# Kernel tuning notes

Hardware: AMD Instinct MI355X
Metric: run time of the kernel (lower is better)

Reference implementation:

```python
import jax, jax.numpy as jnp
import numpy as np

DIM = 512
H = 8
HD = 64          # hidden_dim = dim // num_heads
TD = 64          # time_dim -> time features = 2*TD = 128
LIN = 1536
EPS = 1e-5

def layer_norm(x, g, b):
    mu = jnp.mean(x, axis=-1, keepdims=True)
    var = jnp.mean((x - mu) ** 2, axis=-1, keepdims=True)
    return (x - mu) * jax.lax.rsqrt(var + EPS) * g + b

def setup_inputs() -> dict:
    key = jax.random.key(0)
    ks = jax.random.split(key, 16)
    B, L = 2, 2048
    return {
        "tensor": jax.random.normal(ks[0], (B, L, DIM), jnp.float32),
        "attention_mask": jnp.ones((B, L), jnp.float32),
        "time_angle": jax.random.uniform(ks[1], (H, TD), jnp.float32),
        "head_time_delta": jax.random.uniform(ks[2], (H,), jnp.float32),
        "Qw": jax.random.normal(ks[3], (DIM, H * HD), jnp.float32) * 0.02,
        "q_bias": jnp.zeros((H * HD,), jnp.float32),
        "Kw": jax.random.normal(ks[4], (DIM, H * HD), jnp.float32) * 0.02,
        "Kb": jax.random.normal(ks[5], (H * HD,), jnp.float32) * 0.02,
        "Vw": jax.random.normal(ks[6], (DIM, H * HD), jnp.float32) * 0.02,
        "Vb": jnp.zeros((H * HD,), jnp.float32),
        "Ow": jax.random.normal(ks[7], (H * HD, DIM), jnp.float32) * 0.02,
        "Ob": jnp.zeros((DIM,), jnp.float32),
        "ln1_g": jnp.ones((DIM,), jnp.float32),
        "ln1_b": jnp.zeros((DIM,), jnp.float32),
        "Win": jax.random.normal(ks[8], (DIM, LIN), jnp.float32) * 0.02,
        "b_in": jax.random.normal(ks[9], (LIN,), jnp.float32) * 0.02,
        "Wout": jax.random.normal(ks[10], (LIN, DIM), jnp.float32) * 0.02,
        "b_out": jnp.zeros((DIM,), jnp.float32),
        "ln2_g": jnp.ones((DIM,), jnp.float32),
        "ln2_b": jnp.zeros((DIM,), jnp.float32),
    }

def reference(tensor, attention_mask, time_angle, head_time_delta, Qw, q_bias,
              Kw, Kb, Vw, Vb, Ow, Ob, ln1_g, ln1_b, Win, b_in, Wout, b_out,
              ln2_g, ln2_b):
    B, L = tensor.shape[:2]
    inv_sqrt = 1.0 / np.sqrt(HD).astype(np.float32)
    # queries: sigmoid-gated scalar weight per (b,l,h)
    q = (tensor @ Qw - jnp.exp(q_bias)).reshape(B, L, H, HD)
    q = jax.nn.sigmoid(q) / HD * attention_mask[..., None, None]  # [B,L,H,HD]
    # time features (note: source reuses time_angles for k_time too)
    t = jnp.arange(L, dtype=tensor.dtype)
    ang = (t[:, None, None] + head_time_delta[None, :, None]) * time_angle  # [L,H,TD]
    c, s = jnp.cos(ang), jnp.sin(ang)
    time = jnp.concatenate([c + s, c - s], axis=-1) * inv_sqrt  # [L,H,2TD]
    qt = q.sum(-1)[..., None] * time                            # [B,L,H,2TD]
    # (K branch is dead code in source: computed but never used)
    attn = jnp.einsum('blhd,thd->blth', qt, time)               # [B,L,L,H]
    v = (tensor @ Vw + Vb).reshape(B, L, H, HD)
    comb = jnp.einsum('blth,bthd->blhd', attn, v)               # [B,L,H,HD]
    attn_out = comb.reshape(B, L, H * HD) @ Ow + Ob
    inter = layer_norm(tensor + attn_out, ln1_g, ln1_b)         # dropout = id (eval)
    lin = jax.nn.gelu(inter @ Win + b_in, approximate=True) @ Wout + b_out
    return layer_norm(inter + lin, ln2_g, ln2_b)
```

## Files before the change

### kernel.cpp

```cpp
#include <hip/hip_runtime.h>
#include <hip/hip_bf16.h>

typedef __hip_bfloat16 bf16;
typedef __attribute__((ext_vector_type(8))) __bf16 bf16x8;
typedef __attribute__((ext_vector_type(4))) float f32x4;

#define DIM   512
#define NH    8
#define HDIM  64
#define LIND  1536
#define LSEQ  2048
#define ROWS  4096
#define TF    128
#define KCH   32

__device__ __forceinline__ float b2f(bf16 v){ return __bfloat162float(v); }
__device__ __forceinline__ void stc(float* C, size_t i, float v){ C[i] = v; }
__device__ __forceinline__ void stc(bf16*  C, size_t i, float v){ C[i] = __float2bfloat16(v); }

typedef const __attribute__((address_space(1))) unsigned int* gp1_t;
typedef __attribute__((address_space(3))) unsigned int* lp3_t;
__device__ __forceinline__ void gload16(const bf16* g, unsigned short* l) {
    __builtin_amdgcn_global_load_lds((gp1_t)(const void*)g, (lp3_t)(void*)l, 16, 0, 0);
}

__global__ __launch_bounds__(256) void setup_kernel(const float* __restrict__ tensor,
                                                    const float* __restrict__ tang,
                                                    const float* __restrict__ htd,
                                                    const float* __restrict__ Qw,
                                                    const float* __restrict__ Vw,
                                                    const float* __restrict__ Ow,
                                                    const float* __restrict__ Win,
                                                    const float* __restrict__ Wout,
                                                    bf16* __restrict__ tensorb,
                                                    bf16* __restrict__ timef,
                                                    bf16* __restrict__ timefT,
                                                    bf16* __restrict__ QwT,
                                                    bf16* __restrict__ VwT,
                                                    bf16* __restrict__ OwT,
                                                    bf16* __restrict__ WinT,
                                                    bf16* __restrict__ WoutT)
{
    int id = blockIdx.x;
    if (id < 2048) {
        int i = id * 256 + threadIdx.x;
        float4 v = ((const float4*)tensor)[i];
        bf16 t[4];
        t[0] = __float2bfloat16(v.x); t[1] = __float2bfloat16(v.y);
        t[2] = __float2bfloat16(v.z); t[3] = __float2bfloat16(v.w);
        *(uint2*)&tensorb[(size_t)i * 4] = *(uint2*)t;
        return;
    }
    if (id < 6144) {
        int idx = (id - 2048) * 256 + threadIdx.x;
        int d = idx & 63;
        int h = (idx >> 6) & 7;
        int l = idx >> 9;
        float ang = ((float)l + htd[h]) * tang[h * 64 + d];
        float s, c;
        sincosf(ang, &s, &c);
        bf16* p = timef + ((size_t)l * NH + h) * TF;
        p[d]      = __float2bfloat16((c + s) * 0.125f);
        p[d + 64] = __float2bfloat16((c - s) * 0.125f);
        return;
    }
    if (id < 10240) {
        int q = id - 6144;
        int h  = q >> 9;
        int rem = q & 511;
        int d  = rem >> 3;
        int l  = (rem & 7) * 256 + threadIdx.x;
        float ang = ((float)l + htd[h]) * tang[h * 64 + d];
        float s, c;
        sincosf(ang, &s, &c);
        timefT[((size_t)(h * 128 + d)) * LSEQ + l]      = __float2bfloat16((c + s) * 0.125f);
        timefT[((size_t)(h * 128 + d + 64)) * LSEQ + l] = __float2bfloat16((c - s) * 0.125f);
        return;
    }
    id -= 10240;
    const float* in; bf16* out; int R, C, tx, ty;
    if (id < 256)        { in = Qw;   out = QwT;   R = 512;  C = 512;  tx = id & 15; ty = id >> 4; }
    else if (id < 512)   { id -= 256;  in = Vw;   out = VwT;   R = 512;  C = 512;  tx = id & 15; ty = id >> 4; }
    else if (id < 768)   { id -= 512;  in = Ow;   out = OwT;   R = 512;  C = 512;  tx = id & 15; ty = id >> 4; }
    else if (id < 1536)  { id -= 768;  in = Win;  out = WinT;  R = 512;  C = 1536; tx = id % 48; ty = id / 48; }
    else                 { id -= 1536; in = Wout; out = WoutT; R = 1536; C = 512;  tx = id & 15; ty = id >> 4; }

    __shared__ float t[32][33];
    int bx = tx * 32, by = ty * 32;
    int x = threadIdx.x & 31, y = threadIdx.x >> 5;
    #pragma unroll
    for (int r = 0; r < 32; r += 8)
        t[y + r][x] = in[(size_t)(by + y + r) * C + bx + x];
    __syncthreads();
    #pragma unroll
    for (int r = 0; r < 32; r += 8)
        out[(size_t)(bx + y + r) * R + by + x] = __float2bfloat16(t[x][y + r]);
}


template<int BM, int BN, int EPI, typename OUTT>
__global__ __launch_bounds__(256) void gemm_big(const bf16* __restrict__ A,
                                                const bf16* __restrict__ Bt,
                                                const float* __restrict__ bias,
                                                const float* __restrict__ res,
                                                OUTT* __restrict__ C,
                                                int M, int N, int K)
{
    constexpr int RM = BM / 32, RN = BN / 32;
    constexpr int ITA = BM / 32, ITB = BN / 32;
    __shared__ unsigned short As[2][BM * 64];
    __shared__ unsigned short Bs[2][BN * 64];

    int tid  = threadIdx.x;
    int lane = tid & 63, wave = tid >> 6;
    int wr = wave >> 1, wc = wave & 1;
    int bm = blockIdx.y * BM, bn = blockIdx.x * BN;
    int l15 = lane & 15, lk = lane >> 4;

    const bf16* gA[ITA]; const bf16* gB[ITB];
    #pragma unroll
    for (int it = 0; it < ITA; ++it) {
        int e = it * 256 + tid, row = e >> 3, g = e & 7;
        gA[it] = &A[(size_t)(bm + row) * K + (g ^ (row & 7)) * 8];
    }
    #pragma unroll
    for (int it = 0; it < ITB; ++it) {
        int e = it * 256 + tid, row = e >> 3, g = e & 7;
        gB[it] = &Bt[(size_t)(bn + row) * K + (g ^ (row & 7)) * 8];
    }

    f32x4 acc[RM][RN] = {};
    int NT = K >> 6;

    #pragma unroll
    for (int it = 0; it < ITA; ++it) gload16(gA[it], &As[0][(it * 256 + tid) * 8]);
    #pragma unroll
    for (int it = 0; it < ITB; ++it) gload16(gB[it], &Bs[0][(it * 256 + tid) * 8]);
    __syncthreads();

    for (int t = 0; t < NT; ++t) {
        int cur = t & 1;
        if (t + 1 < NT) {
            #pragma unroll
            for (int it = 0; it < ITA; ++it)
                gload16(gA[it] + (t + 1) * 64, &As[cur ^ 1][(it * 256 + tid) * 8]);
            #pragma unroll
            for (int it = 0; it < ITB; ++it)
                gload16(gB[it] + (t + 1) * 64, &Bs[cur ^ 1][(it * 256 + tid) * 8]);
        }
        #pragma unroll
        for (int s = 0; s < 2; ++s) {
            bf16x8 a[RM], b[RN];
            int g8 = ((s * 4 + lk) ^ (l15 & 7)) * 8;
            #pragma unroll
            for (int m = 0; m < RM; ++m) {
                int row = wr * (BM / 2) + m * 16 + l15;
                a[m] = *(const bf16x8*)&As[cur][row * 64 + g8];
            }
            #pragma unroll
            for (int n = 0; n < RN; ++n) {
                int row = wc * (BN / 2) + n * 16 + l15;
                b[n] = *(const bf16x8*)&Bs[cur][row * 64 + g8];
            }
            #pragma unroll
            for (int m = 0; m < RM; ++m)
                #pragma unroll
                for (int n = 0; n < RN; ++n)
                    acc[m][n] = __builtin_amdgcn_mfma_f32_16x16x32_bf16(a[m], b[n], acc[m][n], 0, 0, 0);
        }
        __syncthreads();
    }

    #pragma unroll
    for (int m = 0; m < RM; ++m) {
        #pragma unroll
        for (int n = 0; n < RN; ++n) {
            int gcol = bn + wc * (BN / 2) + n * 16 + l15;
            float bs = bias[gcol];
            #pragma unroll
            for (int r = 0; r < 4; ++r) {
                int grow = bm + wr * (BM / 2) + m * 16 + lk * 4 + r;
                float x = acc[m][n][r];
                float o;
                if constexpr (EPI == 2) {
                    o = x + bs + res[(size_t)grow * N + gcol];
                } else if constexpr (EPI == 3) {
                    float t = x + bs;
                    float u = t + 0.044715f * t * t * t;
                    o = 0.5f * t * (1.0f + tanhf(0.7978845608028654f * u));
                } else {
                    o = x + bs + res[(size_t)grow * N + gcol];
                }
                stc(C, (size_t)grow * N + gcol, o);
            }
        }
    }
}

__global__ __launch_bounds__(256) void gemm_qv(const bf16* __restrict__ A,
                                               const bf16* __restrict__ Bt,
                                               const float* __restrict__ qb,
                                               const float* __restrict__ Vb,
                                               float* __restrict__ qs,
                                               bf16* __restrict__ vT)
{
    constexpr int BM = 64, BN = 128, RM = 2, RN = 4;
    __shared__ unsigned short As[2][BM * 64];
    __shared__ unsigned short Bs[2][BN * 64];
    __shared__ float qsums[2][64];

    const int K = DIM;
    int tid  = threadIdx.x;
    int lane = tid & 63, wave = tid >> 6;
    int wr = wave >> 1, wc = wave & 1;
    int bm = blockIdx.y * BM, bn = blockIdx.x * BN;
    int l15 = lane & 15, lk = lane >> 4;

    const bf16* gA[2]; const bf16* gB[4];
    #pragma unroll
    for (int it = 0; it < 2; ++it) {
        int e = it * 256 + tid, row = e >> 3, g = e & 7;
        gA[it] = &A[(size_t)(bm + row) * K + (g ^ (row & 7)) * 8];
    }
    #pragma unroll
    for (int it = 0; it < 4; ++it) {
        int e = it * 256 + tid, row = e >> 3, g = e & 7;
        gB[it] = &Bt[(size_t)(bn + row) * K + (g ^ (row & 7)) * 8];
    }

    f32x4 acc[RM][RN] = {};
    const int NT = K >> 6;

    #pragma unroll
    for (int it = 0; it < 2; ++it) gload16(gA[it], &As[0][(it * 256 + tid) * 8]);
    #pragma unroll
    for (int it = 0; it < 4; ++it) gload16(gB[it], &Bs[0][(it * 256 + tid) * 8]);
    __syncthreads();

    for (int t = 0; t < NT; ++t) {
        int cur = t & 1;
        if (t + 1 < NT) {
            #pragma unroll
            for (int it = 0; it < 2; ++it)
                gload16(gA[it] + (t + 1) * 64, &As[cur ^ 1][(it * 256 + tid) * 8]);
            #pragma unroll
            for (int it = 0; it < 4; ++it)
                gload16(gB[it] + (t + 1) * 64, &Bs[cur ^ 1][(it * 256 + tid) * 8]);
        }
        #pragma unroll
        for (int s = 0; s < 2; ++s) {
            bf16x8 a[RM], b[RN];
            int g8 = ((s * 4 + lk) ^ (l15 & 7)) * 8;
            #pragma unroll
            for (int m = 0; m < RM; ++m) {
                int row = wr * 32 + m * 16 + l15;
                a[m] = *(const bf16x8*)&As[cur][row * 64 + g8];
            }
            #pragma unroll
            for (int n = 0; n < RN; ++n) {
                int row = wc * 64 + n * 16 + l15;
                b[n] = *(const bf16x8*)&Bs[cur][row * 64 + g8];
            }
            #pragma unroll
            for (int m = 0; m < RM; ++m)
                #pragma unroll
                for (int n = 0; n < RN; ++n)
                    acc[m][n] = __builtin_amdgcn_mfma_f32_16x16x32_bf16(a[m], b[n], acc[m][n], 0, 0, 0);
        }
        __syncthreads();
    }

    if (bn < DIM) {
        float eq[RN];
        #pragma unroll
        for (int n = 0; n < RN; ++n)
            eq[n] = expf(qb[bn + wc * 64 + n * 16 + l15]);
        #pragma unroll
        for (int m = 0; m < RM; ++m) {
            #pragma unroll
            for (int r = 0; r < 4; ++r) {
                float s = 0.f;
                #pragma unroll
                for (int n = 0; n < RN; ++n) {
                    float x = acc[m][n][r] - eq[n];
                    s += 1.0f / (1.0f + expf(-x));
                }
                s *= (1.0f / 64.0f);
                #pragma unroll
                for (int off = 1; off < 16; off <<= 1) s += __shfl_xor(s, off);
                if (l15 == 0)
                    qsums[wc][wr * 32 + m * 16 + lk * 4 + r] = s;
            }
        }
        __syncthreads();
        if (tid < 128) {
            int hh = tid >> 6, row = tid & 63;
            qs[(size_t)(bm + row) * NH + (bn >> 6) + hh] = qsums[hh][row];
        }
    } else {
        #pragma unroll
        for (int m = 0; m < RM; ++m) {
            int grow0 = bm + wr * 32 + m * 16 + lk * 4;
            #pragma unroll
            for (int n = 0; n < RN; ++n) {
                int gcol = bn - DIM + wc * 64 + n * 16 + l15;
                float bs = Vb[gcol];
                bf16 tmp[4];
                #pragma unroll
                for (int r = 0; r < 4; ++r)
                    tmp[r] = __float2bfloat16(acc[m][n][r] + bs);
                *(uint2*)&vT[(size_t)gcol * ROWS + grow0] = *(uint2*)tmp;
            }
        }
    }
}

__global__ __launch_bounds__(256) void wpart_mfma(const bf16* __restrict__ timefT,
                                                  const bf16* __restrict__ vT,
                                                  float* __restrict__ wpart)
{
    __shared__ unsigned short As[128 * 64];
    __shared__ unsigned short Bs[64 * 64];

    int bh = blockIdx.x;
    int kc = blockIdx.y;
    int b = bh >> 3, h = bh & 7;
    int tid  = threadIdx.x;
    int lane = tid & 63, wave = tid >> 6;
    int wr = wave >> 1, wc = wave & 1;
    int l15 = lane & 15, lk = lane >> 4;
    int k0 = kc * 64;

    const bf16* Abase = timefT + (size_t)h * (128 * LSEQ) + k0;
    const bf16* Bbase = vT + (size_t)h * 64 * ROWS + (size_t)b * LSEQ + k0;

    #pragma unroll
    for (int it = 0; it < 4; ++it) {
        int e = it * 256 + tid, row = e >> 3, g = e & 7;
        gload16(Abase + (size_t)row * LSEQ + (g ^ (row & 7)) * 8, &As[e * 8]);
    }
    #pragma unroll
    for (int it = 0; it < 2; ++it) {
        int e = it * 256 + tid, row = e >> 3, g = e & 7;
        gload16(Bbase + (size_t)row * ROWS + (g ^ (row & 7)) * 8, &Bs[e * 8]);
    }
    __syncthreads();

    f32x4 acc[4][2] = {};
    #pragma unroll
    for (int s = 0; s < 2; ++s) {
        bf16x8 a[4], bv[2];
        int g8 = ((s * 4 + lk) ^ (l15 & 7)) * 8;
        #pragma unroll
        for (int m = 0; m < 4; ++m) {
            int row = wr * 64 + m * 16 + l15;
            a[m] = *(const bf16x8*)&As[row * 64 + g8];
        }
        #pragma unroll
        for (int n = 0; n < 2; ++n) {
            int row = wc * 32 + n * 16 + l15;
            bv[n] = *(const bf16x8*)&Bs[row * 64 + g8];
        }
        #pragma unroll
        for (int m = 0; m < 4; ++m)
            #pragma unroll
            for (int n = 0; n < 2; ++n)
                acc[m][n] = __builtin_amdgcn_mfma_f32_16x16x32_bf16(a[m], bv[n], acc[m][n], 0, 0, 0);
    }

    float* wp = wpart + ((size_t)(kc * 16 + bh)) * (HDIM * TF);
    #pragma unroll
    for (int m = 0; m < 4; ++m) {
        int gd0 = wr * 64 + m * 16 + lk * 4;
        #pragma unroll
        for (int n = 0; n < 2; ++n) {
            int ghd = wc * 32 + n * 16 + l15;
            *(f32x4*)&wp[ghd * TF + gd0] = acc[m][n];
        }
    }
}

__global__ __launch_bounds__(256) void wred_kernel(const float* __restrict__ wpart,
                                                   bf16* __restrict__ WT)
{
    int i = blockIdx.x * 256 + threadIdx.x;
    float s = 0.f;
    #pragma unroll
    for (int kc = 0; kc < KCH; ++kc)
        s += wpart[(size_t)kc * 131072 + i];
    WT[i] = __float2bfloat16(s);
}

__global__ __launch_bounds__(256) void comb_mfma(const bf16* __restrict__ timef,
                                                 const bf16* __restrict__ WT,
                                                 const float* __restrict__ qs,
                                                 const float* __restrict__ mask,
                                                 bf16* __restrict__ comb)
{
    int bh = blockIdx.x;
    int b = bh >> 3, h = bh & 7;
    int lane = threadIdx.x & 63, wave = threadIdx.x >> 6;
    int l15 = lane & 15, lk = lane >> 4;
    int lbase = blockIdx.y * 128 + wave * 32;

    const bf16* wt = WT + (size_t)bh * (HDIM * TF);

    f32x4 acc[2][4] = {};
    #pragma unroll
    for (int ks = 0; ks < 4; ++ks) {
        int kt = ks * 32;
        bf16x8 a[2], bf[4];
        #pragma unroll
        for (int m = 0; m < 2; ++m) {
            int l = lbase + m * 16 + l15;
            a[m] = *(const bf16x8*)&timef[((size_t)l * NH + h) * TF + kt + lk * 8];
        }
        #pragma unroll
        for (int n = 0; n < 4; ++n)
            bf[n] = *(const bf16x8*)&wt[(size_t)(n * 16 + l15) * TF + kt + lk * 8];
        #pragma unroll
        for (int m = 0; m < 2; ++m)
            #pragma unroll
            for (int n = 0; n < 4; ++n)
                acc[m][n] = __builtin_amdgcn_mfma_f32_16x16x32_bf16(a[m], bf[n], acc[m][n], 0, 0, 0);
    }

    #pragma unroll
    for (int m = 0; m < 2; ++m) {
        #pragma unroll
        for (int r = 0; r < 4; ++r) {
            int l = lbase + m * 16 + lk * 4 + r;
            int row = b * LSEQ + l;
            float q = qs[(size_t)row * NH + h] * mask[row];
            #pragma unroll
            for (int n = 0; n < 4; ++n) {
                int hd = n * 16 + l15;
                comb[(size_t)row * DIM + h * HDIM + hd] =
                    __float2bfloat16(q * acc[m][n][r]);
            }
        }
    }
}

template<int WB>
__global__ __launch_bounds__(256) void ln_kernel(const float* __restrict__ X,
                                                 const float* __restrict__ g,
                                                 const float* __restrict__ bta,
                                                 float* __restrict__ outf,
                                                 bf16* __restrict__ outb)
{
    int row = blockIdx.x;
    const float* x = X + (size_t)row * DIM;
    float v0 = x[threadIdx.x], v1 = x[threadIdx.x + 256];
    float s = v0 + v1, s2 = v0 * v0 + v1 * v1;
    #pragma unroll
    for (int off = 1; off < 64; off <<= 1) {
        s  += __shfl_xor(s,  off);
        s2 += __shfl_xor(s2, off);
    }
    __shared__ float sh[2][4];
    int wave = threadIdx.x >> 6, lane = threadIdx.x & 63;
    if (lane == 0) { sh[0][wave] = s; sh[1][wave] = s2; }
    __syncthreads();
    s  = sh[0][0] + sh[0][1] + sh[0][2] + sh[0][3];
    s2 = sh[1][0] + sh[1][1] + sh[1][2] + sh[1][3];
    float mu  = s * (1.0f / DIM);
    float var = s2 * (1.0f / DIM) - mu * mu;
    float inv = rsqrtf(var + 1e-5f);
    int c0 = threadIdx.x, c1 = threadIdx.x + 256;
    float o0 = (v0 - mu) * inv * g[c0] + bta[c0];
    float o1 = (v1 - mu) * inv * g[c1] + bta[c1];
    outf[(size_t)row * DIM + c0] = o0;
    outf[(size_t)row * DIM + c1] = o1;
    if constexpr (WB) {
        outb[(size_t)row * DIM + c0] = __float2bfloat16(o0);
        outb[(size_t)row * DIM + c1] = __float2bfloat16(o1);
    }
}

extern "C" void kernel_launch(void* const* d_in, const int* in_sizes, int n_in,
                              void* d_out, int out_size, void* d_ws, size_t ws_size,
                              hipStream_t stream)
{
    const float* tensor = (const float*)d_in[0];
    const float* mask   = (const float*)d_in[1];
    const float* tang   = (const float*)d_in[2];
    const float* htd    = (const float*)d_in[3];
    const float* Qw     = (const float*)d_in[4];
    const float* qb     = (const float*)d_in[5];
    const float* Vw     = (const float*)d_in[8];
    const float* Vb     = (const float*)d_in[9];
    const float* Ow     = (const float*)d_in[10];
    const float* Ob     = (const float*)d_in[11];
    const float* g1     = (const float*)d_in[12];
    const float* b1     = (const float*)d_in[13];
    const float* Win    = (const float*)d_in[14];
    const float* bin    = (const float*)d_in[15];
    const float* Wout   = (const float*)d_in[16];
    const float* bout   = (const float*)d_in[17];
    const float* g2     = (const float*)d_in[18];
    const float* b2     = (const float*)d_in[19];
    float* out = (float*)d_out;

    float* ws = (float*)d_ws;
    bf16*  vT     = (bf16*)(ws + 0);
    bf16*  actb   = (bf16*)(ws + 0);
    bf16*  tensorb= (bf16*)(ws + 1048576);
    bf16*  combb  = tensorb;
    bf16*  timefb = (bf16*)(ws + 2097152);
    bf16*  timefT = (bf16*)(ws + 3145728);
    bf16*  interb = (bf16*)(ws + 3145728);
    float* wpart  = ws + 4194304;
    float* preLN1 = ws + 4194304;
    float* buf5   = ws + 6291456;
    float* inter  = ws + 8388608;
    bf16*  WTb    = (bf16*)(ws + 10485760);
    float* qs     = ws + 10551296;
    bf16*  QVwT   = (bf16*)(ws + 10584064);
    bf16*  QwT    = QVwT;
    bf16*  VwT    = QVwT + (size_t)512 * 512;
    bf16*  OwT    = (bf16*)(ws + 10846208);
    bf16*  WinT   = (bf16*)(ws + 10977280);
    bf16*  WoutT  = (bf16*)(ws + 11370496);

    setup_kernel<<<12544, 256, 0, stream>>>(tensor, tang, htd, Qw, Vw, Ow, Win, Wout,
                                            tensorb, timefb, timefT, QwT, VwT, OwT, WinT, WoutT);
    gemm_qv<<<dim3(8, 64), 256, 0, stream>>>(tensorb, QVwT, qb, Vb, qs, vT);
    wpart_mfma<<<dim3(16, KCH), 256, 0, stream>>>(timefT, vT, wpart);
    wred_kernel<<<512, 256, 0, stream>>>(wpart, WTb);
    comb_mfma<<<dim3(16, 16), 256, 0, stream>>>(timefb, WTb, qs, mask, combb);
    gemm_big<64, 64, 2, float><<<dim3(8, 64), 256, 0, stream>>>(combb, OwT, Ob, tensor, preLN1, ROWS, DIM, DIM);
    ln_kernel<1><<<ROWS, 256, 0, stream>>>(preLN1, g1, b1, inter, interb);
    gemm_big<64, 128, 3, bf16><<<dim3(12, 64), 256, 0, stream>>>(interb, WinT, bin, nullptr, actb, ROWS, LIND, DIM);
    gemm_big<64, 64, 4, float><<<dim3(8, 64), 256, 0, stream>>>(actb, WoutT, bout, inter, buf5, ROWS, DIM, LIND);
    ln_kernel<0><<<ROWS, 256, 0, stream>>>(buf5, g2, b2, out, nullptr);
}
```

Measured before the change: 101.2 us.

## Compute time features once with LDS transpose, stage vT stores, drop fp32 inter

```diff
diff --git a/kernel.cpp b/kernel.cpp
--- a/kernel.cpp
+++ b/kernel.cpp
@@ -17,6 +17,8 @@
 __device__ __forceinline__ float b2f(bf16 v){ return __bfloat162float(v); }
 __device__ __forceinline__ void stc(float* C, size_t i, float v){ C[i] = v; }
 __device__ __forceinline__ void stc(bf16*  C, size_t i, float v){ C[i] = __float2bfloat16(v); }
+__device__ __forceinline__ float ldr(const float* p, size_t i){ return p[i]; }
+__device__ __forceinline__ float ldr(const bf16*  p, size_t i){ return b2f(p[i]); }
 
 typedef const __attribute__((address_space(1))) unsigned int* gp1_t;
 typedef __attribute__((address_space(3))) unsigned int* lp3_t;
@@ -41,43 +43,54 @@
                                                     bf16* __restrict__ WinT,
                                                     bf16* __restrict__ WoutT)
 {
+    __shared__ unsigned short st0[32][33];
+    __shared__ unsigned short st1[32][33];
+    __shared__ float t[32][33];
+
     int id = blockIdx.x;
     if (id < 2048) {
         int i = id * 256 + threadIdx.x;
         float4 v = ((const float4*)tensor)[i];
-        bf16 t[4];
-        t[0] = __float2bfloat16(v.x); t[1] = __float2bfloat16(v.y);
-        t[2] = __float2bfloat16(v.z); t[3] = __float2bfloat16(v.w);
-        *(uint2*)&tensorb[(size_t)i * 4] = *(uint2*)t;
+        bf16 tt[4];
+        tt[0] = __float2bfloat16(v.x); tt[1] = __float2bfloat16(v.y);
+        tt[2] = __float2bfloat16(v.z); tt[3] = __float2bfloat16(v.w);
+        *(uint2*)&tensorb[(size_t)i * 4] = *(uint2*)tt;
         return;
     }
-    if (id < 6144) {
-        int idx = (id - 2048) * 256 + threadIdx.x;
-        int d = idx & 63;
-        int h = (idx >> 6) & 7;
-        int l = idx >> 9;
-        float ang = ((float)l + htd[h]) * tang[h * 64 + d];
-        float s, c;
-        sincosf(ang, &s, &c);
-        bf16* p = timef + ((size_t)l * NH + h) * TF;
-        p[d]      = __float2bfloat16((c + s) * 0.125f);
-        p[d + 64] = __float2bfloat16((c - s) * 0.125f);
+    if (id < 3072) {
+        int q = id - 2048;
+        int h = q >> 7;
+        int dblk = (q >> 6) & 1;
+        int lblk = q & 63;
+        int d0 = dblk * 32, l0 = lblk * 32;
+        int x = threadIdx.x & 31, y = threadIdx.x >> 5;
+        float ta = tang[h * 64 + d0 + x];
+        float hb = htd[h];
+        #pragma unroll
+        for (int r = 0; r < 4; ++r) {
+            int ll = y + 8 * r;
+            float ang = ((float)(l0 + ll) + hb) * ta;
+            float s, c;
+            sincosf(ang, &s, &c);
+            bf16 v0 = __float2bfloat16((c + s) * 0.125f);
+            bf16 v1 = __float2bfloat16((c - s) * 0.125f);
+            bf16* p = timef + ((size_t)(l0 + ll) * NH + h) * TF;
+            p[d0 + x]      = v0;
+            p[d0 + x + 64] = v1;
+            st0[x][ll] = *(unsigned short*)&v0;
+            st1[x][ll] = *(unsigned short*)&v1;
+        }
+        __syncthreads();
+        #pragma unroll
+        for (int r = 0; r < 4; ++r) {
+            int dd = y + 8 * r;
+            unsigned short u0 = st0[dd][x], u1 = st1[dd][x];
+            timefT[((size_t)(h * 128 + d0 + dd)) * LSEQ + l0 + x]      = *(bf16*)&u0;
+            timefT[((size_t)(h * 128 + d0 + dd + 64)) * LSEQ + l0 + x] = *(bf16*)&u1;
+        }
         return;
     }
-    if (id < 10240) {
-        int q = id - 6144;
-        int h  = q >> 9;
-        int rem = q & 511;
-        int d  = rem >> 3;
-        int l  = (rem & 7) * 256 + threadIdx.x;
-        float ang = ((float)l + htd[h]) * tang[h * 64 + d];
-        float s, c;
-        sincosf(ang, &s, &c);
-        timefT[((size_t)(h * 128 + d)) * LSEQ + l]      = __float2bfloat16((c + s) * 0.125f);
-        timefT[((size_t)(h * 128 + d + 64)) * LSEQ + l] = __float2bfloat16((c - s) * 0.125f);
-        return;
-    }
-    id -= 10240;
+    id -= 3072;
     const float* in; bf16* out; int R, C, tx, ty;
     if (id < 256)        { in = Qw;   out = QwT;   R = 512;  C = 512;  tx = id & 15; ty = id >> 4; }
     else if (id < 512)   { id -= 256;  in = Vw;   out = VwT;   R = 512;  C = 512;  tx = id & 15; ty = id >> 4; }
@@ -85,7 +98,6 @@
     else if (id < 1536)  { id -= 768;  in = Win;  out = WinT;  R = 512;  C = 1536; tx = id % 48; ty = id / 48; }
     else                 { id -= 1536; in = Wout; out = WoutT; R = 1536; C = 512;  tx = id & 15; ty = id >> 4; }
 
-    __shared__ float t[32][33];
     int bx = tx * 32, by = ty * 32;
     int x = threadIdx.x & 31, y = threadIdx.x >> 5;
     #pragma unroll
@@ -97,12 +109,11 @@
         out[(size_t)(bx + y + r) * R + by + x] = __float2bfloat16(t[x][y + r]);
 }
 
-
-template<int BM, int BN, int EPI, typename OUTT>
+template<int BM, int BN, int EPI, typename OUTT, typename REST>
 __global__ __launch_bounds__(256) void gemm_big(const bf16* __restrict__ A,
                                                 const bf16* __restrict__ Bt,
                                                 const float* __restrict__ bias,
-                                                const float* __restrict__ res,
+                                                const REST* __restrict__ res,
                                                 OUTT* __restrict__ C,
                                                 int M, int N, int K)
 {
@@ -183,13 +194,13 @@
                 float x = acc[m][n][r];
                 float o;
                 if constexpr (EPI == 2) {
-                    o = x + bs + res[(size_t)grow * N + gcol];
+                    o = x + bs + ldr(res, (size_t)grow * N + gcol);
                 } else if constexpr (EPI == 3) {
                     float t = x + bs;
                     float u = t + 0.044715f * t * t * t;
                     o = 0.5f * t * (1.0f + tanhf(0.7978845608028654f * u));
                 } else {
-                    o = x + bs + res[(size_t)grow * N + gcol];
+                    o = x + bs + ldr(res, (size_t)grow * N + gcol);
                 }
                 stc(C, (size_t)grow * N + gcol, o);
             }
@@ -298,19 +309,29 @@
             qs[(size_t)(bm + row) * NH + (bn >> 6) + hh] = qsums[hh][row];
         }
     } else {
+        unsigned short* tb = &Bs[0][0];
         #pragma unroll
         for (int m = 0; m < RM; ++m) {
-            int grow0 = bm + wr * 32 + m * 16 + lk * 4;
+            int trow0 = wr * 32 + m * 16 + lk * 4;
             #pragma unroll
             for (int n = 0; n < RN; ++n) {
-                int gcol = bn - DIM + wc * 64 + n * 16 + l15;
-                float bs = Vb[gcol];
+                int col = wc * 64 + n * 16 + l15;
+                float bs = Vb[bn - DIM + col];
                 bf16 tmp[4];
                 #pragma unroll
                 for (int r = 0; r < 4; ++r)
                     tmp[r] = __float2bfloat16(acc[m][n][r] + bs);
-                *(uint2*)&vT[(size_t)gcol * ROWS + grow0] = *(uint2*)tmp;
-            }
+                *(uint2*)&tb[col * 72 + trow0] = *(uint2*)tmp;
+            }
+        }
+        __syncthreads();
+        #pragma unroll
+        for (int rep = 0; rep < 8; ++rep) {
+            int idx = rep * 256 + tid;
+            int col = idx >> 4;
+            int t4  = (idx & 15) * 4;
+            uint2 v = *(uint2*)&tb[col * 72 + t4];
+            *(uint2*)&vT[(size_t)(bn - DIM + col) * ROWS + bm + t4] = v;
         }
     }
 }
@@ -442,7 +463,7 @@
     }
 }
 
-template<int WB>
+template<int OUTBF>
 __global__ __launch_bounds__(256) void ln_kernel(const float* __restrict__ X,
                                                  const float* __restrict__ g,
                                                  const float* __restrict__ bta,
@@ -470,11 +491,12 @@
     int c0 = threadIdx.x, c1 = threadIdx.x + 256;
     float o0 = (v0 - mu) * inv * g[c0] + bta[c0];
     float o1 = (v1 - mu) * inv * g[c1] + bta[c1];
-    outf[(size_t)row * DIM + c0] = o0;
-    outf[(size_t)row * DIM + c1] = o1;
-    if constexpr (WB) {
+    if constexpr (OUTBF) {
         outb[(size_t)row * DIM + c0] = __float2bfloat16(o0);
         outb[(size_t)row * DIM + c1] = __float2bfloat16(o1);
+    } else {
+        outf[(size_t)row * DIM + c0] = o0;
+        outf[(size_t)row * DIM + c1] = o1;
     }
 }
 
@@ -513,25 +535,24 @@
     float* wpart  = ws + 4194304;
     float* preLN1 = ws + 4194304;
     float* buf5   = ws + 6291456;
-    float* inter  = ws + 8388608;
-    bf16*  WTb    = (bf16*)(ws + 10485760);
-    float* qs     = ws + 10551296;
-    bf16*  QVwT   = (bf16*)(ws + 10584064);
+    bf16*  WTb    = (bf16*)(ws + 8388608);
+    float* qs     = ws + 8454144;
+    bf16*  QVwT   = (bf16*)(ws + 8486912);
     bf16*  QwT    = QVwT;
     bf16*  VwT    = QVwT + (size_t)512 * 512;
-    bf16*  OwT    = (bf16*)(ws + 10846208);
-    bf16*  WinT   = (bf16*)(ws + 10977280);
-    bf16*  WoutT  = (bf16*)(ws + 11370496);
-
-    setup_kernel<<<12544, 256, 0, stream>>>(tensor, tang, htd, Qw, Vw, Ow, Win, Wout,
-                                            tensorb, timefb, timefT, QwT, VwT, OwT, WinT, WoutT);
+    bf16*  OwT    = (bf16*)(ws + 8749056);
+    bf16*  WinT   = (bf16*)(ws + 8880128);
+    bf16*  WoutT  = (bf16*)(ws + 9273344);
+
+    setup_kernel<<<5376, 256, 0, stream>>>(tensor, tang, htd, Qw, Vw, Ow, Win, Wout,
+                                           tensorb, timefb, timefT, QwT, VwT, OwT, WinT, WoutT);
     gemm_qv<<<dim3(8, 64), 256, 0, stream>>>(tensorb, QVwT, qb, Vb, qs, vT);
     wpart_mfma<<<dim3(16, KCH), 256, 0, stream>>>(timefT, vT, wpart);
     wred_kernel<<<512, 256, 0, stream>>>(wpart, WTb);
     comb_mfma<<<dim3(16, 16), 256, 0, stream>>>(timefb, WTb, qs, mask, combb);
-    gemm_big<64, 64, 2, float><<<dim3(8, 64), 256, 0, stream>>>(combb, OwT, Ob, tensor, preLN1, ROWS, DIM, DIM);
-    ln_kernel<1><<<ROWS, 256, 0, stream>>>(preLN1, g1, b1, inter, interb);
-    gemm_big<64, 128, 3, bf16><<<dim3(12, 64), 256, 0, stream>>>(interb, WinT, bin, nullptr, actb, ROWS, LIND, DIM);
-    gemm_big<64, 64, 4, float><<<dim3(8, 64), 256, 0, stream>>>(actb, WoutT, bout, inter, buf5, ROWS, DIM, LIND);
+    gemm_big<64, 64, 2, float, float><<<dim3(8, 64), 256, 0, stream>>>(combb, OwT, Ob, tensor, preLN1, ROWS, DIM, DIM);
+    ln_kernel<1><<<ROWS, 256, 0, stream>>>(preLN1, g1, b1, nullptr, interb);
+    gemm_big<64, 128, 3, bf16, float><<<dim3(12, 64), 256, 0, stream>>>(interb, WinT, bin, nullptr, actb, ROWS, LIND, DIM);
+    gemm_big<64, 64, 4, float, bf16><<<dim3(8, 64), 256, 0, stream>>>(actb, WoutT, bout, interb, buf5, ROWS, DIM, LIND);
     ln_kernel<0><<<ROWS, 256, 0, stream>>>(buf5, g2, b2, out, nullptr);
 }
```

New measurement: 98.78 us. 2.4% less time.
